# Performance work log

Hardware: AMD Instinct MI355X
Metric: run time of the kernel (lower is better)

## Reference

```python
import jax, jax.numpy as jnp
import numpy as np

N_TAXA = 32   # N taxa
K = 256       # particles
T = 16        # live subtrees at this step (t = N - r)
R = 16        # merges already done
S = 1024      # alignment sites
A = 4         # DNA alphabet
D = 64        # embedding dim
C = 16        # site-position feature dim
PRIOR_LEN = 0.1


def _expm4(M):
    """Matrix exponential of [..., A, A] via scaling-and-squaring + Taylor."""
    n_sq = 6
    Ms = M / (2.0 ** n_sq)
    I = jnp.eye(M.shape[-1], dtype=M.dtype)
    P = I + Ms
    Tm = Ms
    for i in range(2, 7):
        Tm = jnp.matmul(Tm, Ms) / i
        P = P + Tm
    for _ in range(n_sq):
        P = jnp.matmul(P, P)
    return P


def _stat_probs(emb_ExD, site_SxC, W_stat, W_site):
    # q_matrix_decoder.stat_probs_VxSxA: per-node, per-site stationary probs
    logits = emb_ExD @ W_stat                     # [E, A]
    logits = logits[:, None, :] + site_SxC @ W_site  # [E, S, A]
    return jax.nn.softmax(logits, axis=-1)


def setup_inputs() -> dict:
    key = jax.random.key(0)
    ks = jax.random.split(key, 10)
    ldf = np.zeros(2 * N_TAXA, np.float32)
    for n in range(2, 2 * N_TAXA):
        ldf[n] = ldf[n - 2] + np.log(n)
    return {
        "log_weight_K": jax.random.normal(ks[0], (K,), jnp.float32),
        "branch1_lengths_Kxr": jax.random.uniform(ks[1], (K, R), jnp.float32) * 0.2 + 1e-3,
        "branch2_lengths_Kxr": jax.random.uniform(ks[2], (K, R), jnp.float32) * 0.2 + 1e-3,
        "leaf_counts_Kxt": jnp.ones((K, T), jnp.int32),
        "embeddings_KxtxD": jax.random.normal(ks[3], (K, T, D), jnp.float32),
        "log_felsensteins_KxtxSxA": jax.nn.log_softmax(
            jax.random.normal(ks[4], (K, T, S, A), jnp.float32), axis=-1),
        "log_pi_K": jax.random.normal(ks[5], (K,), jnp.float32),
        "site_positions_SxC": jax.random.uniform(ks[6], (S, C), jnp.float32),
        "W_stat": jax.random.normal(ks[7], (D, A), jnp.float32) * 0.1,
        "W_site": jax.random.normal(ks[8], (C, A), jnp.float32) * 0.1,
        "log_double_factorials_2N": jnp.asarray(ldf),
    }


def reference(log_weight_K, branch1_lengths_Kxr, branch2_lengths_Kxr,
              leaf_counts_Kxt, embeddings_KxtxD, log_felsensteins_KxtxSxA,
              log_pi_K, site_positions_SxC, W_stat, W_site,
              log_double_factorials_2N):
    K_, T_, S_, A_ = log_felsensteins_KxtxSxA.shape
    key = jax.random.key(42)
    kres, ki, koff, ku1, ku2 = jax.random.split(key, 5)

    # ---- SMC categorical resampling over particles ----
    idxK = jax.random.categorical(kres, log_weight_K, shape=(K_,))
    b1r = branch1_lengths_Kxr[idxK]
    b2r = branch2_lengths_Kxr[idxK]
    lc = leaf_counts_Kxt[idxK]
    emb = embeddings_KxtxD[idxK]
    logf = log_felsensteins_KxtxSxA[idxK]
    prev_log_pi = log_pi_K[idxK]

    # ---- proposal (J=1): uniform pair + exponential branch lengths ----
    i = jax.random.randint(ki, (K_,), 0, T_)
    off = jax.random.randint(koff, (K_,), 1, T_)
    j = (i + off) % T_
    idx1 = jnp.minimum(i, j)
    idx2 = jnp.maximum(i, j)
    branch1 = -PRIOR_LEN * jnp.log(jax.random.uniform(ku1, (K_,), minval=1e-6, maxval=1.0))
    branch2 = -PRIOR_LEN * jnp.log(jax.random.uniform(ku2, (K_,), minval=1e-6, maxval=1.0))
    ar = jnp.arange(K_)
    new_emb = 0.5 * (emb[ar, idx1] + emb[ar, idx2])  # [K, D]
    log_v_plus = jnp.log(T_ * (T_ - 1) / 2.0)        # log #pairs

    # ---- merge: put merged value at idx1, move last slot into idx2, drop last ----
    def merge(arr, new_val):
        arr = arr.at[ar, idx1].set(new_val)
        arr = arr.at[ar, idx2].set(arr[ar, T_ - 1])
        return arr[:, :T_ - 1]

    lc_new = merge(lc, lc[ar, idx1] + lc[ar, idx2])   # [K, t-1]
    emb_new = merge(emb, new_emb)                     # [K, t-1, D]

    # ---- Felsenstein pruning step for the merged node ----
    stat = _stat_probs(new_emb, site_positions_SxC, W_stat, W_site)  # [K,S,A]
    Q = jnp.broadcast_to(stat[:, :, None, :], (K_, S_, A_, A_)) - jnp.eye(A_, dtype=stat.dtype)
    P1 = _expm4(Q * branch1[:, None, None, None])  # [K,S,A,A]
    P2 = _expm4(Q * branch2[:, None, None, None])
    f1 = jnp.exp(logf[ar, idx1])  # [K,S,A]
    f2 = jnp.exp(logf[ar, idx2])
    new_logf = (jnp.log(jnp.einsum('ksab,ksb->ksa', P1, f1) + 1e-30)
                + jnp.log(jnp.einsum('ksab,ksb->ksa', P2, f2) + 1e-30))
    logf_new = merge(logf, new_logf)  # [K, t-1, S, A]

    # ---- log pi over the forest: per-subtree likelihood + priors ----
    t_new = T_ - 1
    stat_all = _stat_probs(emb_new.reshape(K_ * t_new, -1), site_positions_SxC,
                           W_stat, W_site).reshape(K_, t_new, S_, A_)
    log_stat = jnp.log(stat_all)
    L = jnp.sum(jax.scipy.special.logsumexp(logf_new + log_stat, axis=-1), axis=-1)  # [K,t-1]
    topo_idx = jnp.clip(2 * lc_new - 3, 0, 2 * N_TAXA - 1)
    topo = -log_double_factorials_2N[topo_idx] * (lc_new >= 2).astype(L.dtype)
    b1_all = jnp.concatenate([b1r, branch1[:, None]], axis=1)  # [K, r+1]
    b2_all = jnp.concatenate([b2r, branch2[:, None]], axis=1)
    prior = (jnp.sum(-b1_all / PRIOR_LEN, axis=1) + jnp.sum(-b2_all / PRIOR_LEN, axis=1)
             - 2.0 * (b1_all.shape[1]) * jnp.log(jnp.asarray(PRIOR_LEN, L.dtype)))
    log_pi_new = jnp.sum(L + topo, axis=1) + prior

    # ---- importance weight ----
    log_v_minus = jnp.log(jnp.maximum(jnp.sum((lc_new > 1).astype(L.dtype), axis=1), 1.0))
    log_weight_new = log_pi_new - prev_log_pi + log_v_minus - log_v_plus
    return log_weight_new
```

## Files before the change

kernel.cpp:

```cpp
#include <hip/hip_runtime.h>
#include <stdint.h>


#define TF_ROT(x0,x1,r) { x0 += x1; x1 = ((x1<<(r))|(x1>>(32-(r)))); x1 ^= x0; }

__host__ __device__ inline void tf2x32(uint32_t k0, uint32_t k1,
                                       uint32_t x0, uint32_t x1,
                                       uint32_t& o0, uint32_t& o1) {
  uint32_t ks2 = k0 ^ k1 ^ 0x1BD11BDAu;
  x0 += k0; x1 += k1;
  TF_ROT(x0,x1,13) TF_ROT(x0,x1,15) TF_ROT(x0,x1,26) TF_ROT(x0,x1,6)
  x0 += k1; x1 += ks2 + 1u;
  TF_ROT(x0,x1,17) TF_ROT(x0,x1,29) TF_ROT(x0,x1,16) TF_ROT(x0,x1,24)
  x0 += ks2; x1 += k0 + 2u;
  TF_ROT(x0,x1,13) TF_ROT(x0,x1,15) TF_ROT(x0,x1,26) TF_ROT(x0,x1,6)
  x0 += k0; x1 += k1 + 3u;
  TF_ROT(x0,x1,17) TF_ROT(x0,x1,29) TF_ROT(x0,x1,16) TF_ROT(x0,x1,24)
  x0 += k1; x1 += ks2 + 4u;
  TF_ROT(x0,x1,13) TF_ROT(x0,x1,15) TF_ROT(x0,x1,26) TF_ROT(x0,x1,6)
  x0 += ks2; x1 += k0 + 5u;
  o0 = x0; o1 = x1;
}

struct Keys {
  uint32_t kres0, kres1;
  uint32_t k2i0, k2i1;
  uint32_t k1o0, k1o1;
  uint32_t k2o0, k2o1;
  uint32_t ku10, ku11;
  uint32_t ku20, ku21;
};

__device__ inline uint32_t rb_fold(uint32_t k0, uint32_t k1, uint32_t i) {
  uint32_t o0, o1;
  tf2x32(k0, k1, 0u, i, o0, o1);
  return o0 ^ o1;
}

__device__ inline float u01f(uint32_t b) {
  return __uint_as_float((b >> 9) | 0x3F800000u) - 1.0f;
}

#define TINYF 1.17549435e-38f

__global__ __launch_bounds__(256) void k_pre(const float* __restrict__ site,
                                             const float* __restrict__ Wsite,
                                             float* __restrict__ eslw,
                                             int* __restrict__ used) {
  int tid = threadIdx.x;
  int s = blockIdx.x * 256 + tid;
  if (blockIdx.x == 0) used[tid] = 0;
  float a0 = 0.f, a1 = 0.f, a2 = 0.f, a3 = 0.f;
#pragma unroll
  for (int c = 0; c < 16; c++) {
    float sc = site[s * 16 + c];
    a0 += sc * Wsite[c * 4 + 0];
    a1 += sc * Wsite[c * 4 + 1];
    a2 += sc * Wsite[c * 4 + 2];
    a3 += sc * Wsite[c * 4 + 3];
  }
  float4 v; v.x = __expf(a0); v.y = __expf(a1); v.z = __expf(a2); v.w = __expf(a3);
  ((float4*)eslw)[s] = v;
}

__global__ __launch_bounds__(256) void k_setup(
    const float* __restrict__ logw, const float* __restrict__ b1r,
    const float* __restrict__ b2r, const int* __restrict__ lc,
    const float* __restrict__ emb, const float* __restrict__ logpi,
    const float* __restrict__ Wstat, const float* __restrict__ ldf,
    float* __restrict__ enlm, float* __restrict__ w1w, float* __restrict__ w2w,
    float* __restrict__ cw, int* __restrict__ pw, int* __restrict__ i1w,
    int* __restrict__ i2w, int* __restrict__ used, Keys kk) {
  int k = blockIdx.x, tid = threadIdx.x;
  __shared__ float sval[256];
  __shared__ int   sidx[256];
  __shared__ int   sh_i1, sh_i2;

  {
    uint32_t b = rb_fold(kk.kres0, kk.kres1, (uint32_t)(k * 256 + tid));
    float u = fmaxf(TINYF, u01f(b) + TINYF);
    float g = -logf(-logf(u));
    sval[tid] = g + logw[tid];
    sidx[tid] = tid;
  }
  __syncthreads();
  for (int st = 128; st > 0; st >>= 1) {
    if (tid < st) {
      float va = sval[tid], vb = sval[tid + st];
      int ia = sidx[tid], ib = sidx[tid + st];
      if (vb > va || (vb == va && ib < ia)) { sval[tid] = vb; sidx[tid] = ib; }
    }
    __syncthreads();
  }
  int p = sidx[0];

  if (tid == 0) {
    used[p] = 1;
    uint32_t i = rb_fold(kk.k2i0, kk.k2i1, (uint32_t)k) & 15u;
    uint32_t h = rb_fold(kk.k1o0, kk.k1o1, (uint32_t)k) % 15u;
    uint32_t l = rb_fold(kk.k2o0, kk.k2o1, (uint32_t)k) % 15u;
    uint32_t off = 1u + (h + l) % 15u;
    uint32_t j = (i + off) & 15u;
    int i1 = (int)(i < j ? i : j);
    int i2 = (int)(i < j ? j : i);
    sh_i1 = i1; sh_i2 = i2;

    const float SUBR = 1.0f - 1e-6f;
    float u1 = fmaxf(1e-6f, u01f(rb_fold(kk.ku10, kk.ku11, (uint32_t)k)) * SUBR + 1e-6f);
    float u2 = fmaxf(1e-6f, u01f(rb_fold(kk.ku20, kk.ku21, (uint32_t)k)) * SUBR + 1e-6f);
    float b1 = -0.1f * logf(u1);
    float b2 = -0.1f * logf(u2);
    w1w[k] = 1.0f - expf(-b1);
    w2w[k] = 1.0f - expf(-b2);
    i1w[k] = i1; i2w[k] = i2; pw[k] = p;

    float sb = b1 + b2;
    for (int r = 0; r < 16; r++) sb += b1r[p * 16 + r] + b2r[p * 16 + r];
    float prior = -sb / 0.1f - 34.0f * logf(0.1f);

    float topo_sum = 0.0f; int cnt = 0;
    for (int t = 0; t < 15; t++) {
      int lct;
      if (t == i1)      lct = lc[p * 16 + i1] + lc[p * 16 + i2];
      else if (t == i2) lct = lc[p * 16 + 15];
      else              lct = lc[p * 16 + t];
      int ti = 2 * lct - 3; ti = ti < 0 ? 0 : (ti > 63 ? 63 : ti);
      if (lct >= 2) topo_sum -= ldf[ti];
      if (lct > 1) cnt++;
    }
    float log_v_minus = logf(fmaxf((float)cnt, 1.0f));
    float log_v_plus = logf(120.0f);
    cw[k] = prior + topo_sum - logpi[p] + log_v_minus - log_v_plus;
  }
  __syncthreads();

  if (tid < 4) {
    int a = tid, i1 = sh_i1, i2 = sh_i2, p2 = sidx[0];
    const float* e1 = emb + ((size_t)p2 * 16 + i1) * 64;
    const float* e2 = emb + ((size_t)p2 * 16 + i2) * 64;
    float acc = 0.0f;
    for (int d = 0; d < 64; d++) acc += 0.5f * (e1[d] + e2[d]) * Wstat[d * 4 + a];
    enlm[k * 4 + a] = __expf(acc);
  }
}

__global__ __launch_bounds__(256) void k_lorig(
    const float* __restrict__ lfg, const float* __restrict__ eslw,
    const float* __restrict__ emb, const float* __restrict__ Wstat,
    const int* __restrict__ used, float* __restrict__ Lpart) {
  int p = blockIdx.y, sblk = blockIdx.x, tid = threadIdx.x;
  if (used[p] == 0) return;
  __shared__ float enl[64];
  __shared__ float sred[16 * 4];
  if (tid < 64) {
    int t = tid >> 2, a = tid & 3;
    const float4* e4 = (const float4*)(emb + ((size_t)p * 16 + t) * 64);
    float acc = 0.0f;
#pragma unroll
    for (int d4 = 0; d4 < 16; d4++) {
      float4 e = e4[d4];
      acc += e.x * Wstat[(d4 * 4 + 0) * 4 + a] + e.y * Wstat[(d4 * 4 + 1) * 4 + a] +
             e.z * Wstat[(d4 * 4 + 2) * 4 + a] + e.w * Wstat[(d4 * 4 + 3) * 4 + a];
    }
    enl[tid] = __expf(acc);
  }
  __syncthreads();
  int s = sblk * 256 + tid;
  const float4 esl = ((const float4*)eslw)[s];
  const float* base = lfg + (size_t)p * 65536;

  float acc[16];
#pragma unroll
  for (int t = 0; t < 16; t++) {
    float4 lf = *(const float4*)(base + t * 4096 + s * 4);
    float w0 = enl[t * 4 + 0] * esl.x, w1 = enl[t * 4 + 1] * esl.y;
    float w2 = enl[t * 4 + 2] * esl.z, w3 = enl[t * 4 + 3] * esl.w;
    float S1 = w0 + w1 + w2 + w3;
    float S2 = __expf(lf.x) * w0 + __expf(lf.y) * w1 +
               __expf(lf.z) * w2 + __expf(lf.w) * w3;
    acc[t] = __log2f(S2) - __log2f(S1);
  }
#pragma unroll
  for (int t = 0; t < 16; t++) {
    float v = acc[t];
    for (int o = 32; o > 0; o >>= 1) v += __shfl_down(v, o, 64);
    if ((tid & 63) == 0) sred[t * 4 + (tid >> 6)] = v;
  }
  __syncthreads();
  if (tid < 16) {
    float s4 = sred[tid * 4 + 0] + sred[tid * 4 + 1] + sred[tid * 4 + 2] + sred[tid * 4 + 3];
    Lpart[((size_t)p * 4 + sblk) * 16 + tid] = s4 * 0.69314718056f;
  }
}

__global__ __launch_bounds__(1024) void k_fin(
    const float* __restrict__ lfg, const float* __restrict__ eslw,
    const float* __restrict__ enlm, const float* __restrict__ w1w,
    const float* __restrict__ w2w, const int* __restrict__ pw,
    const int* __restrict__ i1w, const int* __restrict__ i2w,
    const float* __restrict__ cw, const float* __restrict__ Lpart,
    float* __restrict__ out) {
  int k = blockIdx.x, tid = threadIdx.x;
  __shared__ float sred[16];
  int p = pw[k], i1 = i1w[k], i2 = i2w[k];
  float w1 = w1w[k], w2 = w2w[k];
  float om1 = 1.0f - w1, om2 = 1.0f - w2;
  float m0 = enlm[k * 4 + 0], m1 = enlm[k * 4 + 1];
  float m2 = enlm[k * 4 + 2], m3 = enlm[k * 4 + 3];
  const float* base = lfg + (size_t)p * 65536;

  int s = tid;
  const float4 esl = ((const float4*)eslw)[s];
  float t0 = m0 * esl.x, t1 = m1 * esl.y, t2 = m2 * esl.z, t3 = m3 * esl.w;
  float T = t0 + t1 + t2 + t3;
  float invT = 1.0f / T;
  float4 lf1 = *(const float4*)(base + i1 * 4096 + s * 4);
  float4 lf2 = *(const float4*)(base + i2 * 4096 + s * 4);
  float f10 = __expf(lf1.x), f11 = __expf(lf1.y), f12 = __expf(lf1.z), f13 = __expf(lf1.w);
  float f20 = __expf(lf2.x), f21 = __expf(lf2.y), f22 = __expf(lf2.z), f23 = __expf(lf2.w);
  float dot1 = (t0 * f10 + t1 * f11 + t2 * f12 + t3 * f13) * invT;
  float dot2 = (t0 * f20 + t1 * f21 + t2 * f22 + t3 * f23) * invT;
  float n0 = __logf(om1 * f10 + w1 * dot1 + 1e-30f) + __logf(om2 * f20 + w2 * dot2 + 1e-30f);
  float n1 = __logf(om1 * f11 + w1 * dot1 + 1e-30f) + __logf(om2 * f21 + w2 * dot2 + 1e-30f);
  float n2 = __logf(om1 * f12 + w1 * dot1 + 1e-30f) + __logf(om2 * f22 + w2 * dot2 + 1e-30f);
  float n3 = __logf(om1 * f13 + w1 * dot1 + 1e-30f) + __logf(om2 * f23 + w2 * dot2 + 1e-30f);
  float S2 = __expf(n0) * t0 + __expf(n1) * t1 + __expf(n2) * t2 + __expf(n3) * t3;
  float tot = __logf(S2) - __logf(T);

  for (int o = 32; o > 0; o >>= 1) tot += __shfl_down(tot, o, 64);
  if ((tid & 63) == 0) sred[tid >> 6] = tot;
  __syncthreads();
  if (tid < 64) {
    int t = tid & 15;
    float coef = (t == i1 || t == i2) ? 0.0f : 1.0f;
    float v = coef * Lpart[(size_t)p * 64 + tid];
    if (tid < 16) v += sred[tid];
    for (int o = 32; o > 0; o >>= 1) v += __shfl_down(v, o, 64);
    if (tid == 0) out[k] = cw[k] + v;
  }
}

extern "C" void kernel_launch(void* const* d_in, const int* in_sizes, int n_in,
                              void* d_out, int out_size, void* d_ws, size_t ws_size,
                              hipStream_t stream) {
  const float* logw  = (const float*)d_in[0];
  const float* b1r   = (const float*)d_in[1];
  const float* b2r   = (const float*)d_in[2];
  const int*   lc    = (const int*)d_in[3];
  const float* emb   = (const float*)d_in[4];
  const float* lfg   = (const float*)d_in[5];
  const float* logpi = (const float*)d_in[6];
  const float* site  = (const float*)d_in[7];
  const float* Wstat = (const float*)d_in[8];
  const float* Wsite = (const float*)d_in[9];
  const float* ldf   = (const float*)d_in[10];

  char* w = (char*)d_ws;
  float* eslw  = (float*)w; w += 1024 * 4 * 4;
  float* enlm  = (float*)w; w += 256 * 4 * 4;
  float* w1w   = (float*)w; w += 256 * 4;
  float* w2w   = (float*)w; w += 256 * 4;
  float* cw    = (float*)w; w += 256 * 4;
  int*   pw    = (int*)w;   w += 256 * 4;
  int*   i1w   = (int*)w;   w += 256 * 4;
  int*   i2w   = (int*)w;   w += 256 * 4;
  int*   used  = (int*)w;   w += 256 * 4;
  float* Lpart = (float*)w; w += 256 * 64 * 4;

  uint32_t S0[5], S1[5];
  for (uint32_t i = 0; i < 5; i++) tf2x32(0u, 42u, 0u, i, S0[i], S1[i]);
  Keys kk;
  kk.kres0 = S0[0]; kk.kres1 = S1[0];
  kk.ku10  = S0[3]; kk.ku11  = S1[3];
  kk.ku20  = S0[4]; kk.ku21  = S1[4];
  {
    uint32_t a0, a1, b0, b1;
    tf2x32(S0[1], S1[1], 0u, 0u, a0, a1);
    tf2x32(S0[1], S1[1], 0u, 1u, b0, b1);
    (void)a0; (void)a1;
    kk.k2i0 = b0; kk.k2i1 = b1;
  }
  {
    uint32_t a0, a1, b0, b1;
    tf2x32(S0[2], S1[2], 0u, 0u, a0, a1);
    tf2x32(S0[2], S1[2], 0u, 1u, b0, b1);
    kk.k1o0 = a0; kk.k1o1 = a1;
    kk.k2o0 = b0; kk.k2o1 = b1;
  }

  k_pre<<<4, 256, 0, stream>>>(site, Wsite, eslw, used);
  k_setup<<<256, 256, 0, stream>>>(logw, b1r, b2r, lc, emb, logpi, Wstat, ldf,
                                   enlm, w1w, w2w, cw, pw, i1w, i2w, used, kk);
  dim3 gC(4, 256);
  k_lorig<<<gC, 256, 0, stream>>>(lfg, eslw, emb, Wstat, used, Lpart);
  k_fin<<<256, 1024, 0, stream>>>(lfg, eslw, enlm, w1w, w2w, pw, i1w, i2w,
                                  cw, Lpart, (float*)d_out);
}
```

Before: 129.6 us.

## Fuse pre, setup, per-parent likelihood and final kernels into one launch

Collapses the four kernels into a single 1024-thread-per-particle kernel. Each block now does parent resampling, computes site and embedding weights, sums all 16 subtree likelihoods for its resampled parent, handles the merged subtree and writes the output, with intermediates kept in shared memory instead of workspace. This removes three launch boundaries and the global round-trips between kernels. In exchange, the per-parent likelihood work is no longer deduplicated: a parent picked by several particles is recomputed once per particle.

```diff
diff --git a/kernel.cpp b/kernel.cpp
--- a/kernel.cpp
+++ b/kernel.cpp
@@ -43,40 +43,24 @@
 
 #define TINYF 1.17549435e-38f
 
-__global__ __launch_bounds__(256) void k_pre(const float* __restrict__ site,
-                                             const float* __restrict__ Wsite,
-                                             float* __restrict__ eslw,
-                                             int* __restrict__ used) {
-  int tid = threadIdx.x;
-  int s = blockIdx.x * 256 + tid;
-  if (blockIdx.x == 0) used[tid] = 0;
-  float a0 = 0.f, a1 = 0.f, a2 = 0.f, a3 = 0.f;
-#pragma unroll
-  for (int c = 0; c < 16; c++) {
-    float sc = site[s * 16 + c];
-    a0 += sc * Wsite[c * 4 + 0];
-    a1 += sc * Wsite[c * 4 + 1];
-    a2 += sc * Wsite[c * 4 + 2];
-    a3 += sc * Wsite[c * 4 + 3];
-  }
-  float4 v; v.x = __expf(a0); v.y = __expf(a1); v.z = __expf(a2); v.w = __expf(a3);
-  ((float4*)eslw)[s] = v;
-}
-
-__global__ __launch_bounds__(256) void k_setup(
+__global__ __launch_bounds__(1024) void k_all(
     const float* __restrict__ logw, const float* __restrict__ b1r,
     const float* __restrict__ b2r, const int* __restrict__ lc,
-    const float* __restrict__ emb, const float* __restrict__ logpi,
-    const float* __restrict__ Wstat, const float* __restrict__ ldf,
-    float* __restrict__ enlm, float* __restrict__ w1w, float* __restrict__ w2w,
-    float* __restrict__ cw, int* __restrict__ pw, int* __restrict__ i1w,
-    int* __restrict__ i2w, int* __restrict__ used, Keys kk) {
+    const float* __restrict__ emb, const float* __restrict__ lfg,
+    const float* __restrict__ logpi, const float* __restrict__ site,
+    const float* __restrict__ Wstat, const float* __restrict__ Wsite,
+    const float* __restrict__ ldf, float* __restrict__ out, Keys kk) {
   int k = blockIdx.x, tid = threadIdx.x;
   __shared__ float sval[256];
   __shared__ int   sidx[256];
+  __shared__ float enl[64];
+  __shared__ float sredt[256];
+  __shared__ float sredm[16];
+  __shared__ float sh_m[4];
+  __shared__ float sh_w1, sh_w2, sh_cw;
   __shared__ int   sh_i1, sh_i2;
 
-  {
+  if (tid < 256) {
     uint32_t b = rb_fold(kk.kres0, kk.kres1, (uint32_t)(k * 256 + tid));
     float u = fmaxf(TINYF, u01f(b) + TINYF);
     float g = -logf(-logf(u));
@@ -94,8 +78,36 @@
   }
   int p = sidx[0];
 
-  if (tid == 0) {
-    used[p] = 1;
+  float es0, es1, es2, es3;
+  {
+    int s = tid;
+    float a0 = 0.f, a1 = 0.f, a2 = 0.f, a3 = 0.f;
+#pragma unroll
+    for (int c = 0; c < 16; c++) {
+      float sc = site[s * 16 + c];
+      a0 += sc * Wsite[c * 4 + 0];
+      a1 += sc * Wsite[c * 4 + 1];
+      a2 += sc * Wsite[c * 4 + 2];
+      a3 += sc * Wsite[c * 4 + 3];
+    }
+    es0 = __expf(a0); es1 = __expf(a1); es2 = __expf(a2); es3 = __expf(a3);
+  }
+
+  if (tid >= 64 && tid < 128) {
+    int q = tid - 64;
+    int t = q >> 2, a = q & 3;
+    const float4* e4 = (const float4*)(emb + ((size_t)p * 16 + t) * 64);
+    float acc = 0.0f;
+#pragma unroll
+    for (int d4 = 0; d4 < 16; d4++) {
+      float4 e = e4[d4];
+      acc += e.x * Wstat[(d4 * 4 + 0) * 4 + a] + e.y * Wstat[(d4 * 4 + 1) * 4 + a] +
+             e.z * Wstat[(d4 * 4 + 2) * 4 + a] + e.w * Wstat[(d4 * 4 + 3) * 4 + a];
+    }
+    enl[q] = __expf(acc);
+  }
+
+  if (tid < 5) {
     uint32_t i = rb_fold(kk.k2i0, kk.k2i1, (uint32_t)k) & 15u;
     uint32_t h = rb_fold(kk.k1o0, kk.k1o1, (uint32_t)k) % 15u;
     uint32_t l = rb_fold(kk.k2o0, kk.k2o1, (uint32_t)k) % 15u;
@@ -103,78 +115,53 @@
     uint32_t j = (i + off) & 15u;
     int i1 = (int)(i < j ? i : j);
     int i2 = (int)(i < j ? j : i);
-    sh_i1 = i1; sh_i2 = i2;
-
-    const float SUBR = 1.0f - 1e-6f;
-    float u1 = fmaxf(1e-6f, u01f(rb_fold(kk.ku10, kk.ku11, (uint32_t)k)) * SUBR + 1e-6f);
-    float u2 = fmaxf(1e-6f, u01f(rb_fold(kk.ku20, kk.ku21, (uint32_t)k)) * SUBR + 1e-6f);
-    float b1 = -0.1f * logf(u1);
-    float b2 = -0.1f * logf(u2);
-    w1w[k] = 1.0f - expf(-b1);
-    w2w[k] = 1.0f - expf(-b2);
-    i1w[k] = i1; i2w[k] = i2; pw[k] = p;
-
-    float sb = b1 + b2;
-    for (int r = 0; r < 16; r++) sb += b1r[p * 16 + r] + b2r[p * 16 + r];
-    float prior = -sb / 0.1f - 34.0f * logf(0.1f);
-
-    float topo_sum = 0.0f; int cnt = 0;
-    for (int t = 0; t < 15; t++) {
-      int lct;
-      if (t == i1)      lct = lc[p * 16 + i1] + lc[p * 16 + i2];
-      else if (t == i2) lct = lc[p * 16 + 15];
-      else              lct = lc[p * 16 + t];
-      int ti = 2 * lct - 3; ti = ti < 0 ? 0 : (ti > 63 ? 63 : ti);
-      if (lct >= 2) topo_sum -= ldf[ti];
-      if (lct > 1) cnt++;
-    }
-    float log_v_minus = logf(fmaxf((float)cnt, 1.0f));
-    float log_v_plus = logf(120.0f);
-    cw[k] = prior + topo_sum - logpi[p] + log_v_minus - log_v_plus;
+
+    if (tid < 4) {
+      if (tid == 0) { sh_i1 = i1; sh_i2 = i2; }
+      int a = tid;
+      const float* e1p = emb + ((size_t)p * 16 + i1) * 64;
+      const float* e2p = emb + ((size_t)p * 16 + i2) * 64;
+      float acc = 0.0f;
+      for (int d = 0; d < 64; d++) acc += 0.5f * (e1p[d] + e2p[d]) * Wstat[d * 4 + a];
+      sh_m[a] = __expf(acc);
+    } else {
+      const float SUBR = 1.0f - 1e-6f;
+      float u1 = fmaxf(1e-6f, u01f(rb_fold(kk.ku10, kk.ku11, (uint32_t)k)) * SUBR + 1e-6f);
+      float u2 = fmaxf(1e-6f, u01f(rb_fold(kk.ku20, kk.ku21, (uint32_t)k)) * SUBR + 1e-6f);
+      float b1 = -0.1f * logf(u1);
+      float b2 = -0.1f * logf(u2);
+      sh_w1 = 1.0f - expf(-b1);
+      sh_w2 = 1.0f - expf(-b2);
+
+      float sb = b1 + b2;
+      for (int r = 0; r < 16; r++) sb += b1r[p * 16 + r] + b2r[p * 16 + r];
+      float prior = -sb / 0.1f - 34.0f * logf(0.1f);
+
+      float topo_sum = 0.0f; int cnt = 0;
+      for (int t = 0; t < 15; t++) {
+        int lct;
+        if (t == i1)      lct = lc[p * 16 + i1] + lc[p * 16 + i2];
+        else if (t == i2) lct = lc[p * 16 + 15];
+        else              lct = lc[p * 16 + t];
+        int ti = 2 * lct - 3; ti = ti < 0 ? 0 : (ti > 63 ? 63 : ti);
+        if (lct >= 2) topo_sum -= ldf[ti];
+        if (lct > 1) cnt++;
+      }
+      float log_v_minus = logf(fmaxf((float)cnt, 1.0f));
+      float log_v_plus = logf(120.0f);
+      sh_cw = prior + topo_sum - logpi[p] + log_v_minus - log_v_plus;
+    }
   }
   __syncthreads();
 
-  if (tid < 4) {
-    int a = tid, i1 = sh_i1, i2 = sh_i2, p2 = sidx[0];
-    const float* e1 = emb + ((size_t)p2 * 16 + i1) * 64;
-    const float* e2 = emb + ((size_t)p2 * 16 + i2) * 64;
-    float acc = 0.0f;
-    for (int d = 0; d < 64; d++) acc += 0.5f * (e1[d] + e2[d]) * Wstat[d * 4 + a];
-    enlm[k * 4 + a] = __expf(acc);
-  }
-}
-
-__global__ __launch_bounds__(256) void k_lorig(
-    const float* __restrict__ lfg, const float* __restrict__ eslw,
-    const float* __restrict__ emb, const float* __restrict__ Wstat,
-    const int* __restrict__ used, float* __restrict__ Lpart) {
-  int p = blockIdx.y, sblk = blockIdx.x, tid = threadIdx.x;
-  if (used[p] == 0) return;
-  __shared__ float enl[64];
-  __shared__ float sred[16 * 4];
-  if (tid < 64) {
-    int t = tid >> 2, a = tid & 3;
-    const float4* e4 = (const float4*)(emb + ((size_t)p * 16 + t) * 64);
-    float acc = 0.0f;
-#pragma unroll
-    for (int d4 = 0; d4 < 16; d4++) {
-      float4 e = e4[d4];
-      acc += e.x * Wstat[(d4 * 4 + 0) * 4 + a] + e.y * Wstat[(d4 * 4 + 1) * 4 + a] +
-             e.z * Wstat[(d4 * 4 + 2) * 4 + a] + e.w * Wstat[(d4 * 4 + 3) * 4 + a];
-    }
-    enl[tid] = __expf(acc);
-  }
-  __syncthreads();
-  int s = sblk * 256 + tid;
-  const float4 esl = ((const float4*)eslw)[s];
   const float* base = lfg + (size_t)p * 65536;
-
+  int s = tid;
   float acc[16];
 #pragma unroll
   for (int t = 0; t < 16; t++) {
     float4 lf = *(const float4*)(base + t * 4096 + s * 4);
-    float w0 = enl[t * 4 + 0] * esl.x, w1 = enl[t * 4 + 1] * esl.y;
-    float w2 = enl[t * 4 + 2] * esl.z, w3 = enl[t * 4 + 3] * esl.w;
+    float w0 = enl[t * 4 + 0] * es0, w1 = enl[t * 4 + 1] * es1;
+    float w2 = enl[t * 4 + 2] * es2, w3 = enl[t * 4 + 3] * es3;
     float S1 = w0 + w1 + w2 + w3;
     float S2 = __expf(lf.x) * w0 + __expf(lf.y) * w1 +
                __expf(lf.z) * w2 + __expf(lf.w) * w3;
@@ -184,59 +171,46 @@
   for (int t = 0; t < 16; t++) {
     float v = acc[t];
     for (int o = 32; o > 0; o >>= 1) v += __shfl_down(v, o, 64);
-    if ((tid & 63) == 0) sred[t * 4 + (tid >> 6)] = v;
+    if ((tid & 63) == 0) sredt[t * 16 + (tid >> 6)] = v;
+  }
+
+  {
+    int i1 = sh_i1, i2 = sh_i2;
+    float w1 = sh_w1, w2 = sh_w2;
+    float om1 = 1.0f - w1, om2 = 1.0f - w2;
+    float m0 = sh_m[0], m1 = sh_m[1], m2 = sh_m[2], m3 = sh_m[3];
+    float t0 = m0 * es0, t1 = m1 * es1, t2 = m2 * es2, t3 = m3 * es3;
+    float T = t0 + t1 + t2 + t3;
+    float invT = 1.0f / T;
+    float4 lf1 = *(const float4*)(base + i1 * 4096 + s * 4);
+    float4 lf2 = *(const float4*)(base + i2 * 4096 + s * 4);
+    float f10 = __expf(lf1.x), f11 = __expf(lf1.y), f12 = __expf(lf1.z), f13 = __expf(lf1.w);
+    float f20 = __expf(lf2.x), f21 = __expf(lf2.y), f22 = __expf(lf2.z), f23 = __expf(lf2.w);
+    float dot1 = (t0 * f10 + t1 * f11 + t2 * f12 + t3 * f13) * invT;
+    float dot2 = (t0 * f20 + t1 * f21 + t2 * f22 + t3 * f23) * invT;
+    float n0 = __logf(om1 * f10 + w1 * dot1 + 1e-30f) + __logf(om2 * f20 + w2 * dot2 + 1e-30f);
+    float n1 = __logf(om1 * f11 + w1 * dot1 + 1e-30f) + __logf(om2 * f21 + w2 * dot2 + 1e-30f);
+    float n2 = __logf(om1 * f12 + w1 * dot1 + 1e-30f) + __logf(om2 * f22 + w2 * dot2 + 1e-30f);
+    float n3 = __logf(om1 * f13 + w1 * dot1 + 1e-30f) + __logf(om2 * f23 + w2 * dot2 + 1e-30f);
+    float S2 = __expf(n0) * t0 + __expf(n1) * t1 + __expf(n2) * t2 + __expf(n3) * t3;
+    float tot = __logf(S2) - __logf(T);
+
+    for (int o = 32; o > 0; o >>= 1) tot += __shfl_down(tot, o, 64);
+    if ((tid & 63) == 0) sredm[tid >> 6] = tot;
   }
   __syncthreads();
-  if (tid < 16) {
-    float s4 = sred[tid * 4 + 0] + sred[tid * 4 + 1] + sred[tid * 4 + 2] + sred[tid * 4 + 3];
-    Lpart[((size_t)p * 4 + sblk) * 16 + tid] = s4 * 0.69314718056f;
-  }
-}
-
-__global__ __launch_bounds__(1024) void k_fin(
-    const float* __restrict__ lfg, const float* __restrict__ eslw,
-    const float* __restrict__ enlm, const float* __restrict__ w1w,
-    const float* __restrict__ w2w, const int* __restrict__ pw,
-    const int* __restrict__ i1w, const int* __restrict__ i2w,
-    const float* __restrict__ cw, const float* __restrict__ Lpart,
-    float* __restrict__ out) {
-  int k = blockIdx.x, tid = threadIdx.x;
-  __shared__ float sred[16];
-  int p = pw[k], i1 = i1w[k], i2 = i2w[k];
-  float w1 = w1w[k], w2 = w2w[k];
-  float om1 = 1.0f - w1, om2 = 1.0f - w2;
-  float m0 = enlm[k * 4 + 0], m1 = enlm[k * 4 + 1];
-  float m2 = enlm[k * 4 + 2], m3 = enlm[k * 4 + 3];
-  const float* base = lfg + (size_t)p * 65536;
-
-  int s = tid;
-  const float4 esl = ((const float4*)eslw)[s];
-  float t0 = m0 * esl.x, t1 = m1 * esl.y, t2 = m2 * esl.z, t3 = m3 * esl.w;
-  float T = t0 + t1 + t2 + t3;
-  float invT = 1.0f / T;
-  float4 lf1 = *(const float4*)(base + i1 * 4096 + s * 4);
-  float4 lf2 = *(const float4*)(base + i2 * 4096 + s * 4);
-  float f10 = __expf(lf1.x), f11 = __expf(lf1.y), f12 = __expf(lf1.z), f13 = __expf(lf1.w);
-  float f20 = __expf(lf2.x), f21 = __expf(lf2.y), f22 = __expf(lf2.z), f23 = __expf(lf2.w);
-  float dot1 = (t0 * f10 + t1 * f11 + t2 * f12 + t3 * f13) * invT;
-  float dot2 = (t0 * f20 + t1 * f21 + t2 * f22 + t3 * f23) * invT;
-  float n0 = __logf(om1 * f10 + w1 * dot1 + 1e-30f) + __logf(om2 * f20 + w2 * dot2 + 1e-30f);
-  float n1 = __logf(om1 * f11 + w1 * dot1 + 1e-30f) + __logf(om2 * f21 + w2 * dot2 + 1e-30f);
-  float n2 = __logf(om1 * f12 + w1 * dot1 + 1e-30f) + __logf(om2 * f22 + w2 * dot2 + 1e-30f);
-  float n3 = __logf(om1 * f13 + w1 * dot1 + 1e-30f) + __logf(om2 * f23 + w2 * dot2 + 1e-30f);
-  float S2 = __expf(n0) * t0 + __expf(n1) * t1 + __expf(n2) * t2 + __expf(n3) * t3;
-  float tot = __logf(S2) - __logf(T);
-
-  for (int o = 32; o > 0; o >>= 1) tot += __shfl_down(tot, o, 64);
-  if ((tid & 63) == 0) sred[tid >> 6] = tot;
-  __syncthreads();
+
   if (tid < 64) {
-    int t = tid & 15;
+    int t = tid & 15, sb = tid >> 4;
+    int i1 = sh_i1, i2 = sh_i2;
+    float s4 = sredt[t * 16 + sb * 4 + 0] + sredt[t * 16 + sb * 4 + 1] +
+               sredt[t * 16 + sb * 4 + 2] + sredt[t * 16 + sb * 4 + 3];
+    float Lv = s4 * 0.69314718056f;
     float coef = (t == i1 || t == i2) ? 0.0f : 1.0f;
-    float v = coef * Lpart[(size_t)p * 64 + tid];
-    if (tid < 16) v += sred[tid];
+    float v = coef * Lv;
+    if (tid < 16) v += sredm[tid];
     for (int o = 32; o > 0; o >>= 1) v += __shfl_down(v, o, 64);
-    if (tid == 0) out[k] = cw[k] + v;
+    if (tid == 0) out[k] = sh_cw + v;
   }
 }
 
@@ -255,18 +229,6 @@
   const float* Wsite = (const float*)d_in[9];
   const float* ldf   = (const float*)d_in[10];
 
-  char* w = (char*)d_ws;
-  float* eslw  = (float*)w; w += 1024 * 4 * 4;
-  float* enlm  = (float*)w; w += 256 * 4 * 4;
-  float* w1w   = (float*)w; w += 256 * 4;
-  float* w2w   = (float*)w; w += 256 * 4;
-  float* cw    = (float*)w; w += 256 * 4;
-  int*   pw    = (int*)w;   w += 256 * 4;
-  int*   i1w   = (int*)w;   w += 256 * 4;
-  int*   i2w   = (int*)w;   w += 256 * 4;
-  int*   used  = (int*)w;   w += 256 * 4;
-  float* Lpart = (float*)w; w += 256 * 64 * 4;
-
   uint32_t S0[5], S1[5];
   for (uint32_t i = 0; i < 5; i++) tf2x32(0u, 42u, 0u, i, S0[i], S1[i]);
   Keys kk;
@@ -288,11 +250,6 @@
     kk.k2o0 = b0; kk.k2o1 = b1;
   }
 
-  k_pre<<<4, 256, 0, stream>>>(site, Wsite, eslw, used);
-  k_setup<<<256, 256, 0, stream>>>(logw, b1r, b2r, lc, emb, logpi, Wstat, ldf,
-                                   enlm, w1w, w2w, cw, pw, i1w, i2w, used, kk);
-  dim3 gC(4, 256);
-  k_lorig<<<gC, 256, 0, stream>>>(lfg, eslw, emb, Wstat, used, Lpart);
-  k_fin<<<256, 1024, 0, stream>>>(lfg, eslw, enlm, w1w, w2w, pw, i1w, i2w,
-                                  cw, Lpart, (float*)d_out);
-}
+  k_all<<<256, 1024, 0, stream>>>(logw, b1r, b2r, lc, emb, lfg, logpi,
+                                  site, Wstat, Wsite, ldf, (float*)d_out, kk);
+}
```

Result: no change. 131.3 us (+1.3%).
